# Performance work log

Hardware: AMD Instinct MI355X
Metric: run time of the kernel (lower is better)

Reference implementation:

```python
import jax, jax.numpy as jnp
import numpy as np

VOCAB_SIZE = 50000

def setup_inputs() -> dict:
    key = jax.random.key(0)
    # token index sequences: [batch, seq_len], values in [0, vocab)
    x = jax.random.randint(key, (2048, 200), 0, VOCAB_SIZE, dtype=jnp.int64)
    return {"x": x}

def reference(x) -> jnp.ndarray:
    # Faithful to: sum_{l} one_hot(x[b, l], V)  ->  [batch, vocab] count histogram.
    # Implemented as a scatter-add instead of materializing the
    # [batch, seq_len, vocab] one-hot tensor (same math, O(B*L) traffic on the
    # index side plus the [B, V] output).
    B, L = x.shape
    rows = jnp.broadcast_to(jnp.arange(B)[:, None], (B, L))  # [B, L]
    out = jnp.zeros((B, VOCAB_SIZE), dtype=jnp.float32)
    out = out.at[rows, x].add(jnp.float32(1.0))
    return out
```

## Files before the change

kernel.cpp:

```cpp
#include <hip/hip_runtime.h>

#define VOCAB 50000
#define SEQ   200
#define NF4   (VOCAB / 4)

__global__ __launch_bounds__(256) void MultihotEmbedding_16458314678493_kernel(
    const int* __restrict__ x, float* __restrict__ out) {
  const int row = blockIdx.x;
  float* __restrict__ orow = out + (size_t)row * VOCAB;

  float4* __restrict__ o4 = (float4*)orow;
  const float4 z = make_float4(0.f, 0.f, 0.f, 0.f);
  for (int i = threadIdx.x; i < NF4; i += 256) o4[i] = z;
  __syncthreads();

  const int t = threadIdx.x;
  if (t < SEQ) {
    const int idx = x[row * SEQ + t];
    atomicAdd(orow + idx, 1.0f);
  }
}

extern "C" void kernel_launch(void* const* d_in, const int* in_sizes, int n_in,
                              void* d_out, int out_size, void* d_ws, size_t ws_size,
                              hipStream_t stream) {
  const int* x = (const int*)d_in[0];
  float* out = (float*)d_out;
  const int batch = in_sizes[0] / SEQ;
  MultihotEmbedding_16458314678493_kernel<<<batch, 256, 0, stream>>>(x, out);
}
```

Measured before the change: 438.5 us.

## Split zero-fill and scatter into separate grid-stride and per-token kernels

Replaces the per-row fused kernel (zero row, barrier, then atomics) with two launches. The first is a grid-stride float4 zero-fill over the whole output and the second is a per-token atomic scatter. This removes the in-block barrier and the idle threads during the atomic phase. The cost is an extra kernel launch, and the atomics now hit memory written by another kernel, so they may miss cache.

```diff
diff --git a/kernel.cpp b/kernel.cpp
--- a/kernel.cpp
+++ b/kernel.cpp
@@ -2,22 +2,21 @@
 
 #define VOCAB 50000
 #define SEQ   200
-#define NF4   (VOCAB / 4)
 
-__global__ __launch_bounds__(256) void MultihotEmbedding_16458314678493_kernel(
-    const int* __restrict__ x, float* __restrict__ out) {
-  const int row = blockIdx.x;
-  float* __restrict__ orow = out + (size_t)row * VOCAB;
+__global__ __launch_bounds__(256) void MultihotEmbedding_zero_kernel(
+    float4* __restrict__ o4, int n4) {
+  const int stride = gridDim.x * 256;
+  const float4 z = make_float4(0.f, 0.f, 0.f, 0.f);
+  for (int i = blockIdx.x * 256 + threadIdx.x; i < n4; i += stride) o4[i] = z;
+}
 
-  float4* __restrict__ o4 = (float4*)orow;
-  const float4 z = make_float4(0.f, 0.f, 0.f, 0.f);
-  for (int i = threadIdx.x; i < NF4; i += 256) o4[i] = z;
-  __syncthreads();
-
-  const int t = threadIdx.x;
-  if (t < SEQ) {
-    const int idx = x[row * SEQ + t];
-    atomicAdd(orow + idx, 1.0f);
+__global__ __launch_bounds__(256) void MultihotEmbedding_scatter_kernel(
+    const int* __restrict__ x, float* __restrict__ out, int ntok) {
+  const int gid = blockIdx.x * 256 + threadIdx.x;
+  if (gid < ntok) {
+    const int row = gid / SEQ;
+    const int idx = x[gid];
+    atomicAdd(out + (size_t)row * VOCAB + idx, 1.0f);
   }
 }
 
@@ -27,5 +26,11 @@
   const int* x = (const int*)d_in[0];
   float* out = (float*)d_out;
   const int batch = in_sizes[0] / SEQ;
-  MultihotEmbedding_16458314678493_kernel<<<batch, 256, 0, stream>>>(x, out);
+  const int ntok = batch * SEQ;
+  const int n4 = batch * (VOCAB / 4);
+
+  MultihotEmbedding_zero_kernel<<<2048, 256, 0, stream>>>((float4*)out, n4);
+
+  MultihotEmbedding_scatter_kernel<<<(ntok + 255) / 256, 256, 0, stream>>>(
+      x, out, ntok);
 }
```

After: 458.0 us. +4.4%, slower.
